# Kernel tuning notes

Hardware: AMD Instinct MI355X
Metric: run time of the kernel (lower is better)

Reference implementation:

```python
import jax, jax.numpy as jnp
import numpy as np

WARMUP = 5

def _smooth_l1(x):
    a = jnp.abs(x)
    return jnp.where(a < 1.0, 0.5 * a * a, a - 0.5)


def setup_inputs() -> dict:
    key = jax.random.key(0)
    ks = jax.random.split(key, 6)
    B, S, N, M, C = 8, 4, 8192, 50, 10
    return dict(
        pred_boxes=jax.random.normal(ks[0], (B, S, N, 7), jnp.float32),
        pred_classes=jax.random.normal(ks[1], (B, S, N, C), jnp.float32),
        pred_scores=jax.random.normal(ks[2], (B, S, N), jnp.float32),
        gt_boxes=jax.random.normal(ks[3], (B, M, 7), jnp.float32) * 3.0,
        gt_classes=jax.random.randint(ks[4], (B, M), 0, C),
        n_gt=jax.random.randint(ks[5], (B,), 1, M + 1),
        w_center=jnp.float32(2.0),   # loss_weights['center']
        w_obj=jnp.float32(0.5),      # loss_weights['obj']
        w_unmatched=jnp.float32(5.0),# loss_weights['unmatched']
        epoch=0,
    )


def _forward(pred_boxes, pred_classes, pred_scores, gt_boxes, gt_classes, n_gt, w_center, w_obj, w_unmatched, epoch):
    # epoch < WARMUP path: k_factor=10, use_objectness=False, distance_threshold=5.0, cls_weight=0
    K_FACTOR = 10
    COST_THRESH = 5.0 * 10.0  # distance_threshold * 10
    B, S, N, _ = pred_boxes.shape
    M = gt_boxes.shape[1]
    gt_mask = jnp.arange(M)[None, :] < n_gt[:, None]            # [B,M] valid (non-padded) GTs

    pc = pred_boxes[..., :3]                                    # [B,S,N,3]
    gc = gt_boxes[..., :3]                                      # [B,M,3]
    diff = pc[:, :, :, None, :] - gc[:, None, None, :, :]       # [B,S,N,M,3]
    dist = jnp.sqrt(jnp.sum(diff * diff, axis=-1))              # [B,S,N,M] center L2 cost

    # ---- progressive matching (vectorized over B,S,GT) ----
    cost = jnp.where(gt_mask[:, None, None, :], dist, jnp.inf)
    masked = jnp.where(cost < COST_THRESH, cost, jnp.inf)
    neg = -jnp.swapaxes(masked, -1, -2)                         # [B,S,M,N]
    vals, idx = jax.lax.top_k(neg, K_FACTOR)                    # k smallest costs per gt
    pick_ok = vals > -jnp.inf                                   # [B,S,M,k] valid picks
    gt_ids = jnp.broadcast_to(jnp.arange(M, dtype=jnp.int32)[None, None, :, None], idx.shape)
    bidx = jnp.broadcast_to(jnp.arange(B)[:, None, None, None], idx.shape)
    sidx = jnp.broadcast_to(jnp.arange(S)[None, :, None, None], idx.shape)
    assign = jnp.full((B, S, N), -1, dtype=jnp.int32)
    assign = assign.at[bidx, sidx, idx].max(jnp.where(pick_ok, gt_ids, -1))
    matched_gt = pick_ok.any(-1)                                # [B,S,M]
    unmatched = gt_mask[:, None, :] & ~matched_gt               # [B,S,M]

    # ---- center loss (smooth-L1 over matched query/GT center pairs) ----
    pos = assign >= 0                                           # [B,S,N]
    a = jnp.maximum(assign, 0)
    gtc = gc[jnp.arange(B)[:, None, None], a]                   # [B,S,N,3]
    n_pos = pos.sum().astype(jnp.float32)
    loss_center = jnp.sum(_smooth_l1(pc - gtc) * pos[..., None]) / jnp.maximum(n_pos * 3.0, 1.0)

    # ---- progressive objectness loss (BCE-with-logits + dynamic pos_weight) ----
    t = pos.astype(pred_scores.dtype)
    n_neg = jnp.float32(t.size) - n_pos
    pw = jnp.minimum(10.0, n_neg / jnp.maximum(n_pos, 1.0))     # epoch < warmup branch
    x = pred_scores
    loss_obj = jnp.mean(pw * t * jax.nn.softplus(-x) + (1.0 - t) * jax.nn.softplus(x))

    # ---- unmatched-GT loss: pull 5 nearest predictions toward each unmatched GT ----
    dist_t = jnp.swapaxes(dist, -1, -2)                         # [B,S,M,N]
    nd, ni = jax.lax.top_k(-dist_t, 5)
    nd = -nd                                                    # 5 smallest distances [B,S,M,5]
    b5 = jnp.broadcast_to(jnp.arange(B)[:, None, None, None], ni.shape)
    s5 = jnp.broadcast_to(jnp.arange(S)[None, :, None, None], ni.shape)
    obj5 = pred_scores[b5, s5, ni]                              # [B,S,M,5]
    per_gt = jnp.mean(jnp.exp(-nd / 2.0) * (1.0 - obj5), axis=-1)
    per_gt = jnp.where(unmatched, per_gt, 0.0)
    n_entries = jnp.sum(unmatched.any(-1)).astype(jnp.float32)  # number of (b,s) pairs with unmatched gts
    loss_unm = per_gt.sum() / jnp.maximum(n_entries, 1.0)

    return loss_center * w_center + loss_obj * w_obj + loss_unm * w_unmatched


def reference(pred_boxes, pred_classes, pred_scores, gt_boxes, gt_classes, n_gt, w_center, w_obj, w_unmatched, epoch):
    return _forward(pred_boxes, pred_classes, pred_scores, gt_boxes, gt_classes, n_gt, w_center, w_obj, w_unmatched, epoch)
```

## Files before the change

### kernel.cpp

```cpp
#include <hip/hip_runtime.h>

#define NB 8
#define NS 4
#define NN 8192
#define NM 50
#define K10 10
#define COST_THRESH 50.0f
#define LOSS_BLOCKS 256
#define CAP 1024
#define CAP_HI 128
#define TOTAL (NB * NS * NN)
#define TT 512
#define ELEMS (NN / TT)

__device__ __forceinline__ bool lexless(float d1, int i1, float d2, int i2) {
  return (d1 < d2) || (d1 == d2 && i1 < i2);
}

__global__ void __launch_bounds__(256) prep_kernel(
    const float* __restrict__ pred_boxes, float* __restrict__ packed,
    int* __restrict__ assign, float* __restrict__ acc,
    int* __restrict__ bs_unm, int* __restrict__ done) {
  int i = blockIdx.x * blockDim.x + threadIdx.x;
  for (int j = i; j < TOTAL; j += gridDim.x * blockDim.x) {
    assign[j] = -1;
    packed[j] = pred_boxes[j * 7 + 0];
    packed[TOTAL + j] = pred_boxes[j * 7 + 1];
    packed[2 * TOTAL + j] = pred_boxes[j * 7 + 2];
  }
  if (i == 0) { acc[0] = 0.0f; *done = 0; }
  if (i >= 64 && i < 64 + NB * NS) bs_unm[i - 64] = 0;
}

__global__ void __launch_bounds__(TT, 4) topk_kernel(
    const float* __restrict__ packed, const float* __restrict__ pred_scores,
    const float* __restrict__ gt_boxes, const int* __restrict__ n_gt,
    int* __restrict__ assign, float* __restrict__ per_gt_sum,
    int* __restrict__ bs_unm) {
  const int blk = blockIdx.x;
  const int m = blk % NM;
  const int bs = blk / NM;
  const int b = bs / NS;
  const int t = threadIdx.x;
  const int wave = t >> 6;
  const int lane = t & 63;

  __shared__ float scd[CAP];
  __shared__ int sci[CAP];
  __shared__ float sred[2][8];
  __shared__ float sbb[2];
  __shared__ int scount[2][8];
  __shared__ int scnt;
  __shared__ float soutd[K10];
  __shared__ int souti[K10];

  if (t == 0) scnt = 0;

  const float gx = gt_boxes[(b * NM + m) * 7 + 0];
  const float gy = gt_boxes[(b * NM + m) * 7 + 1];
  const float gz = gt_boxes[(b * NM + m) * 7 + 2];
  const bool valid = (m < n_gt[b]);

  const float4* px4 = (const float4*)(packed + (size_t)bs * NN);
  const float4* py4 = (const float4*)(packed + TOTAL + (size_t)bs * NN);
  const float4* pz4 = (const float4*)(packed + 2 * TOTAL + (size_t)bs * NN);

  float d2r[ELEMS];
  float lmin = INFINITY, lmax = 0.0f;
#pragma unroll
  for (int c = 0; c < ELEMS / 4; c++) {
    float4 vx = px4[c * TT + t];
    float4 vy = py4[c * TT + t];
    float4 vz = pz4[c * TT + t];
    float dx, dy, dz;
    dx = vx.x - gx; dy = vy.x - gy; dz = vz.x - gz; d2r[c * 4 + 0] = dx * dx + dy * dy + dz * dz;
    dx = vx.y - gx; dy = vy.y - gy; dz = vz.y - gz; d2r[c * 4 + 1] = dx * dx + dy * dy + dz * dz;
    dx = vx.z - gx; dy = vy.z - gy; dz = vz.z - gz; d2r[c * 4 + 2] = dx * dx + dy * dy + dz * dz;
    dx = vx.w - gx; dy = vy.w - gy; dz = vz.w - gz; d2r[c * 4 + 3] = dx * dx + dy * dy + dz * dz;
#pragma unroll
    for (int j = 0; j < 4; j++) {
      lmin = fminf(lmin, d2r[c * 4 + j]);
      lmax = fmaxf(lmax, d2r[c * 4 + j]);
    }
  }
#pragma unroll
  for (int off = 32; off >= 1; off >>= 1) {
    lmin = fminf(lmin, __shfl_down(lmin, off));
    lmax = fmaxf(lmax, __shfl_down(lmax, off));
  }
  if (lane == 0) { sred[0][wave] = lmin; sred[1][wave] = lmax; }
  __syncthreads();
  if (t == 0) {
    float bmin = INFINITY, bmax = 0.0f;
#pragma unroll
    for (int w = 0; w < TT / 64; w++) {
      bmin = fminf(bmin, sred[0][w]);
      bmax = fmaxf(bmax, sred[1][w]);
    }
    sbb[0] = bmin;
    sbb[1] = bmax;
  }
  __syncthreads();

  float lo = sbb[0];
  float hi = sbb[1] * 1.000001f + 1e-30f;
  float bound = hi;
  int buf = 0;
  for (int iter = 0; iter < 32; iter++) {
    float mid = 0.5f * (lo + hi);
    int c = 0;
#pragma unroll
    for (int e = 0; e < ELEMS; e++) c += (d2r[e] < mid) ? 1 : 0;
#pragma unroll
    for (int off = 32; off >= 1; off >>= 1) c += __shfl_down(c, off);
    if (lane == 0) scount[buf][wave] = c;
    __syncthreads();
    int C = 0;
#pragma unroll
    for (int w = 0; w < TT / 64; w++) C += scount[buf][w];
    buf ^= 1;
    bool collapsed = (mid <= lo) || (mid >= hi);
    if (C >= K10 && (C <= CAP_HI || collapsed)) { bound = mid; break; }
    if (collapsed) { bound = hi; break; }
    if (C < K10) lo = mid; else hi = mid;
  }

#pragma unroll
  for (int e = 0; e < ELEMS; e++) {
    int n = (e < ELEMS ? ((e >> 2) * TT + t) * 4 + (e & 3) : 0);
    bool p = d2r[e] < bound;
    unsigned long long mask = __ballot(p);
    if (mask) {
      int leader = __ffsll((long long)mask) - 1;
      int cnt = __popcll(mask);
      int base = 0;
      if (lane == leader) base = atomicAdd(&scnt, cnt);
      base = __shfl(base, leader);
      int pos = base + __popcll(mask & ((1ull << lane) - 1ull));
      if (p && pos < CAP) { scd[pos] = d2r[e]; sci[pos] = n; }
    }
  }
  __syncthreads();
  const int K = min(scnt, CAP);

  for (int c = t; c < K; c += TT) scd[c] = sqrtf(scd[c]);
  __syncthreads();
  for (int c = t; c < K; c += TT) {
    float dc = scd[c];
    int ic = sci[c];
    int rank = 0;
    for (int o = 0; o < K; o++) rank += lexless(scd[o], sci[o], dc, ic) ? 1 : 0;
    if (rank < K10) { soutd[rank] = dc; souti[rank] = ic; }
  }
  __syncthreads();

  if (t < 64) {
    bool pick = (t < K10) && valid && (soutd[t] < COST_THRESH);
    if (pick) atomicMax(&assign[(size_t)bs * NN + souti[t]], m);
    bool matched = __any(pick);
    if (valid && !matched) {
      float a = 0.0f;
      if (t < 5) a = expf(-0.5f * soutd[t]) * (1.0f - pred_scores[(size_t)bs * NN + souti[t]]);
#pragma unroll
      for (int off = 8; off >= 1; off >>= 1) a += __shfl_down(a, off);
      if (t == 0) {
        atomicAdd(per_gt_sum, a * 0.2f);
        atomicOr(&bs_unm[bs], 1);
      }
    }
  }
}

__global__ void __launch_bounds__(256) loss_final_kernel(
    const float* __restrict__ packed, const float* __restrict__ pred_scores,
    const float* __restrict__ gt_boxes, const int* __restrict__ assign,
    float* __restrict__ partials, int* __restrict__ done,
    const float* __restrict__ acc, const int* __restrict__ bs_unm,
    const float* __restrict__ wc, const float* __restrict__ wo,
    const float* __restrict__ wu, float* __restrict__ out) {
  int tid = blockIdx.x * blockDim.x + threadIdx.x;
  float lc = 0.0f, spp = 0.0f, spn = 0.0f, np = 0.0f;
  for (int i = tid; i < TOTAL; i += gridDim.x * blockDim.x) {
    int a = assign[i];
    float x = pred_scores[i];
    if (a >= 0) {
      np += 1.0f;
      int b = i / (NS * NN);
      const float* gbp = &gt_boxes[(b * NM + a) * 7];
#pragma unroll
      for (int c = 0; c < 3; c++) {
        float diff = packed[c * TOTAL + i] - gbp[c];
        float ad = fabsf(diff);
        lc += (ad < 1.0f) ? 0.5f * ad * ad : (ad - 0.5f);
      }
      spp += log1pf(expf(-fabsf(x))) + fmaxf(-x, 0.0f);
    } else {
      spn += log1pf(expf(-fabsf(x))) + fmaxf(x, 0.0f);
    }
  }
#pragma unroll
  for (int off = 32; off >= 1; off >>= 1) {
    lc += __shfl_down(lc, off);
    spp += __shfl_down(spp, off);
    spn += __shfl_down(spn, off);
    np += __shfl_down(np, off);
  }
  __shared__ float red[4][4];
  __shared__ int s_last;
  int wave = threadIdx.x >> 6;
  if ((threadIdx.x & 63) == 0) {
    red[wave][0] = lc; red[wave][1] = spp; red[wave][2] = spn; red[wave][3] = np;
  }
  __syncthreads();
  if (threadIdx.x == 0) {
    float o0 = 0, o1 = 0, o2 = 0, o3 = 0;
#pragma unroll
    for (int w = 0; w < 4; w++) { o0 += red[w][0]; o1 += red[w][1]; o2 += red[w][2]; o3 += red[w][3]; }
    float* p = &partials[(size_t)blockIdx.x * 8];
    __hip_atomic_store(&p[0], o0, __ATOMIC_RELAXED, __HIP_MEMORY_SCOPE_AGENT);
    __hip_atomic_store(&p[1], o1, __ATOMIC_RELAXED, __HIP_MEMORY_SCOPE_AGENT);
    __hip_atomic_store(&p[2], o2, __ATOMIC_RELAXED, __HIP_MEMORY_SCOPE_AGENT);
    __hip_atomic_store(&p[3], o3, __ATOMIC_RELAXED, __HIP_MEMORY_SCOPE_AGENT);
    __threadfence();
    int ticket = __hip_atomic_fetch_add(done, 1, __ATOMIC_ACQ_REL, __HIP_MEMORY_SCOPE_AGENT);
    s_last = (ticket == gridDim.x - 1) ? 1 : 0;
  }
  __syncthreads();
  if (s_last) {
    __threadfence();
    const int t = threadIdx.x;
    float l0 = __hip_atomic_load(&partials[t * 8 + 0], __ATOMIC_RELAXED, __HIP_MEMORY_SCOPE_AGENT);
    float l1 = __hip_atomic_load(&partials[t * 8 + 1], __ATOMIC_RELAXED, __HIP_MEMORY_SCOPE_AGENT);
    float l2 = __hip_atomic_load(&partials[t * 8 + 2], __ATOMIC_RELAXED, __HIP_MEMORY_SCOPE_AGENT);
    float l3 = __hip_atomic_load(&partials[t * 8 + 3], __ATOMIC_RELAXED, __HIP_MEMORY_SCOPE_AGENT);
#pragma unroll
    for (int off = 32; off >= 1; off >>= 1) {
      l0 += __shfl_down(l0, off);
      l1 += __shfl_down(l1, off);
      l2 += __shfl_down(l2, off);
      l3 += __shfl_down(l3, off);
    }
    __shared__ float red2[4][4];
    if ((t & 63) == 0) {
      red2[t >> 6][0] = l0; red2[t >> 6][1] = l1; red2[t >> 6][2] = l2; red2[t >> 6][3] = l3;
    }
    __syncthreads();
    if (t == 0) {
      float o0 = 0, o1 = 0, o2 = 0, o3 = 0;
#pragma unroll
      for (int w = 0; w < 4; w++) { o0 += red2[w][0]; o1 += red2[w][1]; o2 += red2[w][2]; o3 += red2[w][3]; }
      int ne = 0;
      for (int i = 0; i < NB * NS; i++) ne += bs_unm[i];
      float n_pos = o3;
      float loss_center = o0 / fmaxf(n_pos * 3.0f, 1.0f);
      float n_neg = (float)TOTAL - n_pos;
      float pw = fminf(10.0f, n_neg / fmaxf(n_pos, 1.0f));
      float loss_obj = (pw * o1 + o2) / (float)TOTAL;
      float loss_unm = acc[0] / fmaxf((float)ne, 1.0f);
      out[0] = loss_center * wc[0] + loss_obj * wo[0] + loss_unm * wu[0];
    }
  }
}

extern "C" void kernel_launch(void* const* d_in, const int* in_sizes, int n_in,
                              void* d_out, int out_size, void* d_ws, size_t ws_size,
                              hipStream_t stream) {
  const float* pred_boxes = (const float*)d_in[0];
  const float* pred_scores = (const float*)d_in[2];
  const float* gt_boxes = (const float*)d_in[3];
  const int* n_gt = (const int*)d_in[5];
  const float* wc = (const float*)d_in[6];
  const float* wo = (const float*)d_in[7];
  const float* wu = (const float*)d_in[8];
  float* out = (float*)d_out;

  char* ws = (char*)d_ws;
  int* assign = (int*)ws;
  float* packed = (float*)(ws + (size_t)TOTAL * 4);
  float* acc = (float*)(ws + (size_t)TOTAL * 16);
  int* done = (int*)((char*)acc + 64);
  int* bs_unm = (int*)((char*)acc + 128);
  float* partials = (float*)((char*)acc + 512);

  prep_kernel<<<512, 256, 0, stream>>>(pred_boxes, packed, assign, acc, bs_unm, done);
  topk_kernel<<<NB * NS * NM, TT, 0, stream>>>(packed, pred_scores, gt_boxes,
                                               n_gt, assign, &acc[0], bs_unm);
  loss_final_kernel<<<LOSS_BLOCKS, 256, 0, stream>>>(packed, pred_scores, gt_boxes, assign,
                                                     partials, done, acc, bs_unm, wc, wo, wu, out);
}
```

Baseline: 53.63 us.

## Move assignment to per-(b,s) shared-memory scatter and use galloping threshold search

The top-k kernel now only writes each GT's 10 nearest (distance, index) pairs to a small buffer. The loss kernel runs one block group per (batch, sample) and builds the assignment map in LDS with shared atomics, so the global assign array, its initialisation and the global atomics are gone. The unmatched-GT loss is folded into that kernel. The threshold search now starts from a geometric gallop above the minimum with a looser accept window, and the top-k block shrinks to 256 threads with 32 elements each. The trade-offs are a larger candidate buffer, a possibly bigger rank-sort set, and only 128 loss blocks, each rebuilding the same LDS assignment.

After: 47.49 us. 11.4% less time.

```diff
diff --git a/kernel.cpp b/kernel.cpp
--- a/kernel.cpp
+++ b/kernel.cpp
@@ -6,12 +6,14 @@
 #define NM 50
 #define K10 10
 #define COST_THRESH 50.0f
-#define LOSS_BLOCKS 256
-#define CAP 1024
-#define CAP_HI 128
 #define TOTAL (NB * NS * NN)
-#define TT 512
-#define ELEMS (NN / TT)
+#define TKT 256
+#define TKE 32
+#define CAP 2048
+#define ACCEPT 256
+#define LFT 512
+#define SUBS 4
+#define LF_BLOCKS (NB * NS * SUBS)
 
 __device__ __forceinline__ bool lexless(float d1, int i1, float d2, int i2) {
   return (d1 < d2) || (d1 == d2 && i1 < i2);
@@ -19,24 +21,19 @@
 
 __global__ void __launch_bounds__(256) prep_kernel(
     const float* __restrict__ pred_boxes, float* __restrict__ packed,
-    int* __restrict__ assign, float* __restrict__ acc,
-    int* __restrict__ bs_unm, int* __restrict__ done) {
+    int* __restrict__ done) {
   int i = blockIdx.x * blockDim.x + threadIdx.x;
   for (int j = i; j < TOTAL; j += gridDim.x * blockDim.x) {
-    assign[j] = -1;
     packed[j] = pred_boxes[j * 7 + 0];
     packed[TOTAL + j] = pred_boxes[j * 7 + 1];
     packed[2 * TOTAL + j] = pred_boxes[j * 7 + 2];
   }
-  if (i == 0) { acc[0] = 0.0f; *done = 0; }
-  if (i >= 64 && i < 64 + NB * NS) bs_unm[i - 64] = 0;
-}
-
-__global__ void __launch_bounds__(TT, 4) topk_kernel(
-    const float* __restrict__ packed, const float* __restrict__ pred_scores,
-    const float* __restrict__ gt_boxes, const int* __restrict__ n_gt,
-    int* __restrict__ assign, float* __restrict__ per_gt_sum,
-    int* __restrict__ bs_unm) {
+  if (i == 0) *done = 0;
+}
+
+__global__ void __launch_bounds__(TKT, 4) topk_kernel(
+    const float* __restrict__ packed, const float* __restrict__ gt_boxes,
+    float* __restrict__ outd, int* __restrict__ outi) {
   const int blk = blockIdx.x;
   const int m = blk % NM;
   const int bs = blk / NM;
@@ -47,9 +44,8 @@
 
   __shared__ float scd[CAP];
   __shared__ int sci[CAP];
-  __shared__ float sred[2][8];
-  __shared__ float sbb[2];
-  __shared__ int scount[2][8];
+  __shared__ float sred[2][4];
+  __shared__ int scount[2][4];
   __shared__ int scnt;
   __shared__ float soutd[K10];
   __shared__ int souti[K10];
@@ -59,19 +55,18 @@
   const float gx = gt_boxes[(b * NM + m) * 7 + 0];
   const float gy = gt_boxes[(b * NM + m) * 7 + 1];
   const float gz = gt_boxes[(b * NM + m) * 7 + 2];
-  const bool valid = (m < n_gt[b]);
 
   const float4* px4 = (const float4*)(packed + (size_t)bs * NN);
   const float4* py4 = (const float4*)(packed + TOTAL + (size_t)bs * NN);
   const float4* pz4 = (const float4*)(packed + 2 * TOTAL + (size_t)bs * NN);
 
-  float d2r[ELEMS];
+  float d2r[TKE];
   float lmin = INFINITY, lmax = 0.0f;
 #pragma unroll
-  for (int c = 0; c < ELEMS / 4; c++) {
-    float4 vx = px4[c * TT + t];
-    float4 vy = py4[c * TT + t];
-    float4 vz = pz4[c * TT + t];
+  for (int c = 0; c < TKE / 4; c++) {
+    float4 vx = px4[c * TKT + t];
+    float4 vy = py4[c * TKT + t];
+    float4 vz = pz4[c * TKT + t];
     float dx, dy, dz;
     dx = vx.x - gx; dy = vy.x - gy; dz = vz.x - gz; d2r[c * 4 + 0] = dx * dx + dy * dy + dz * dz;
     dx = vx.y - gx; dy = vy.y - gy; dz = vz.y - gz; d2r[c * 4 + 1] = dx * dx + dy * dy + dz * dz;
@@ -90,44 +85,39 @@
   }
   if (lane == 0) { sred[0][wave] = lmin; sred[1][wave] = lmax; }
   __syncthreads();
-  if (t == 0) {
-    float bmin = INFINITY, bmax = 0.0f;
-#pragma unroll
-    for (int w = 0; w < TT / 64; w++) {
-      bmin = fminf(bmin, sred[0][w]);
-      bmax = fmaxf(bmax, sred[1][w]);
-    }
-    sbb[0] = bmin;
-    sbb[1] = bmax;
-  }
-  __syncthreads();
-
-  float lo = sbb[0];
-  float hi = sbb[1] * 1.000001f + 1e-30f;
-  float bound = hi;
+  const float bmin = fminf(fminf(sred[0][0], sred[0][1]), fminf(sred[0][2], sred[0][3]));
+  const float bmax = fmaxf(fmaxf(sred[1][0], sred[1][1]), fmaxf(sred[1][2], sred[1][3]));
+
+  float lo = bmin;
+  float hi = bmax * 1.000001f + 1e-30f;
+  float g = fmaxf(bmin * 4.0f, 1e-37f);
+  bool have = false;
   int buf = 0;
-  for (int iter = 0; iter < 32; iter++) {
-    float mid = 0.5f * (lo + hi);
+  for (int it = 0; it < 24; it++) {
+    float probe = have ? 0.5f * (lo + hi) : fminf(g, hi);
     int c = 0;
 #pragma unroll
-    for (int e = 0; e < ELEMS; e++) c += (d2r[e] < mid) ? 1 : 0;
+    for (int e = 0; e < TKE; e++) c += (d2r[e] < probe) ? 1 : 0;
 #pragma unroll
     for (int off = 32; off >= 1; off >>= 1) c += __shfl_down(c, off);
     if (lane == 0) scount[buf][wave] = c;
     __syncthreads();
-    int C = 0;
-#pragma unroll
-    for (int w = 0; w < TT / 64; w++) C += scount[buf][w];
+    int C = scount[buf][0] + scount[buf][1] + scount[buf][2] + scount[buf][3];
     buf ^= 1;
-    bool collapsed = (mid <= lo) || (mid >= hi);
-    if (C >= K10 && (C <= CAP_HI || collapsed)) { bound = mid; break; }
-    if (collapsed) { bound = hi; break; }
-    if (C < K10) lo = mid; else hi = mid;
-  }
-
-#pragma unroll
-  for (int e = 0; e < ELEMS; e++) {
-    int n = (e < ELEMS ? ((e >> 2) * TT + t) * 4 + (e & 3) : 0);
+    if (C >= K10) {
+      hi = probe; have = true;
+      if (C <= ACCEPT) break;
+    } else {
+      lo = probe;
+      if (!have) { g *= 4.0f; if (g >= hi) have = true; }
+    }
+    if (have && !(hi > lo + fmaxf(lo, 1e-30f) * 1e-7f)) break;
+  }
+  const float bound = hi;
+
+#pragma unroll
+  for (int e = 0; e < TKE; e++) {
+    int n = ((e >> 2) * TKT + t) * 4 + (e & 3);
     bool p = d2r[e] < bound;
     unsigned long long mask = __ballot(p);
     if (mask) {
@@ -143,9 +133,9 @@
   __syncthreads();
   const int K = min(scnt, CAP);
 
-  for (int c = t; c < K; c += TT) scd[c] = sqrtf(scd[c]);
-  __syncthreads();
-  for (int c = t; c < K; c += TT) {
+  for (int c = t; c < K; c += TKT) scd[c] = sqrtf(scd[c]);
+  __syncthreads();
+  for (int c = t; c < K; c += TKT) {
     float dc = scd[c];
     int ic = sci[c];
     int rank = 0;
@@ -154,42 +144,76 @@
   }
   __syncthreads();
 
-  if (t < 64) {
-    bool pick = (t < K10) && valid && (soutd[t] < COST_THRESH);
-    if (pick) atomicMax(&assign[(size_t)bs * NN + souti[t]], m);
-    bool matched = __any(pick);
-    if (valid && !matched) {
-      float a = 0.0f;
-      if (t < 5) a = expf(-0.5f * soutd[t]) * (1.0f - pred_scores[(size_t)bs * NN + souti[t]]);
-#pragma unroll
-      for (int off = 8; off >= 1; off >>= 1) a += __shfl_down(a, off);
-      if (t == 0) {
-        atomicAdd(per_gt_sum, a * 0.2f);
-        atomicOr(&bs_unm[bs], 1);
-      }
-    }
-  }
-}
-
-__global__ void __launch_bounds__(256) loss_final_kernel(
-    const float* __restrict__ packed, const float* __restrict__ pred_scores,
-    const float* __restrict__ gt_boxes, const int* __restrict__ assign,
+  if (t < K10) {
+    outd[blk * K10 + t] = soutd[t];
+    outi[blk * K10 + t] = souti[t];
+  }
+}
+
+__global__ void __launch_bounds__(LFT) loss_final_kernel(
+    const float* __restrict__ pred_boxes, const float* __restrict__ pred_scores,
+    const float* __restrict__ gt_boxes, const int* __restrict__ n_gt,
+    const float* __restrict__ outd, const int* __restrict__ outi,
     float* __restrict__ partials, int* __restrict__ done,
-    const float* __restrict__ acc, const int* __restrict__ bs_unm,
     const float* __restrict__ wc, const float* __restrict__ wo,
     const float* __restrict__ wu, float* __restrict__ out) {
-  int tid = blockIdx.x * blockDim.x + threadIdx.x;
+  const int blk = blockIdx.x;
+  const int bs = blk / SUBS;
+  const int sub = blk % SUBS;
+  const int b = bs / NS;
+  const int t = threadIdx.x;
+  const int wave = t >> 6;
+
+  __shared__ int lassign[NN];
+  __shared__ int matched[NM];
+  __shared__ float spg;
+  __shared__ int sunm;
+  __shared__ float red[8][4];
+  __shared__ float red2[2][8];
+  __shared__ int s_last;
+
+  for (int i = t; i < NN; i += LFT) lassign[i] = -1;
+  if (t < NM) matched[t] = 0;
+  if (t == 0) { spg = 0.0f; sunm = 0; }
+  const int ngt = n_gt[b];
+  __syncthreads();
+
+  if (t < NM * K10) {
+    int m = t / K10, k = t % K10;
+    if (m < ngt) {
+      float d = outd[(bs * NM + m) * K10 + k];
+      if (d < COST_THRESH) {
+        atomicMax(&lassign[outi[(bs * NM + m) * K10 + k]], m);
+        atomicOr(&matched[m], 1);
+      }
+    }
+  }
+  __syncthreads();
+
+  if (sub == 0 && t < NM && t < ngt && matched[t] == 0) {
+    float a = 0.0f;
+#pragma unroll
+    for (int k = 0; k < 5; k++) {
+      float d = outd[(bs * NM + t) * K10 + k];
+      float sc = pred_scores[(size_t)bs * NN + outi[(bs * NM + t) * K10 + k]];
+      a += expf(-0.5f * d) * (1.0f - sc);
+    }
+    atomicAdd(&spg, a * 0.2f);
+    atomicOr(&sunm, 1);
+  }
+
   float lc = 0.0f, spp = 0.0f, spn = 0.0f, np = 0.0f;
-  for (int i = tid; i < TOTAL; i += gridDim.x * blockDim.x) {
-    int a = assign[i];
-    float x = pred_scores[i];
+  const int base = sub * (NN / SUBS);
+#pragma unroll
+  for (int j = 0; j < NN / SUBS / LFT; j++) {
+    int i = base + t + j * LFT;
+    int a = lassign[i];
+    float x = pred_scores[(size_t)bs * NN + i];
     if (a >= 0) {
       np += 1.0f;
-      int b = i / (NS * NN);
-      const float* gbp = &gt_boxes[(b * NM + a) * 7];
 #pragma unroll
       for (int c = 0; c < 3; c++) {
-        float diff = packed[c * TOTAL + i] - gbp[c];
+        float diff = pred_boxes[((size_t)bs * NN + i) * 7 + c] - gt_boxes[(b * NM + a) * 7 + c];
         float ad = fabsf(diff);
         lc += (ad < 1.0f) ? 0.5f * ad * ad : (ad - 0.5f);
       }
@@ -205,58 +229,57 @@
     spn += __shfl_down(spn, off);
     np += __shfl_down(np, off);
   }
-  __shared__ float red[4][4];
-  __shared__ int s_last;
-  int wave = threadIdx.x >> 6;
-  if ((threadIdx.x & 63) == 0) {
+  if ((t & 63) == 0) {
     red[wave][0] = lc; red[wave][1] = spp; red[wave][2] = spn; red[wave][3] = np;
   }
   __syncthreads();
-  if (threadIdx.x == 0) {
+  if (t == 0) {
     float o0 = 0, o1 = 0, o2 = 0, o3 = 0;
 #pragma unroll
-    for (int w = 0; w < 4; w++) { o0 += red[w][0]; o1 += red[w][1]; o2 += red[w][2]; o3 += red[w][3]; }
-    float* p = &partials[(size_t)blockIdx.x * 8];
+    for (int w = 0; w < 8; w++) { o0 += red[w][0]; o1 += red[w][1]; o2 += red[w][2]; o3 += red[w][3]; }
+    float* p = &partials[(size_t)blk * 8];
     __hip_atomic_store(&p[0], o0, __ATOMIC_RELAXED, __HIP_MEMORY_SCOPE_AGENT);
     __hip_atomic_store(&p[1], o1, __ATOMIC_RELAXED, __HIP_MEMORY_SCOPE_AGENT);
     __hip_atomic_store(&p[2], o2, __ATOMIC_RELAXED, __HIP_MEMORY_SCOPE_AGENT);
     __hip_atomic_store(&p[3], o3, __ATOMIC_RELAXED, __HIP_MEMORY_SCOPE_AGENT);
+    __hip_atomic_store(&p[4], sub == 0 ? spg : 0.0f, __ATOMIC_RELAXED, __HIP_MEMORY_SCOPE_AGENT);
+    __hip_atomic_store(&p[5], sub == 0 ? (float)sunm : 0.0f, __ATOMIC_RELAXED, __HIP_MEMORY_SCOPE_AGENT);
     __threadfence();
     int ticket = __hip_atomic_fetch_add(done, 1, __ATOMIC_ACQ_REL, __HIP_MEMORY_SCOPE_AGENT);
-    s_last = (ticket == gridDim.x - 1) ? 1 : 0;
+    s_last = (ticket == LF_BLOCKS - 1) ? 1 : 0;
   }
   __syncthreads();
   if (s_last) {
     __threadfence();
-    const int t = threadIdx.x;
-    float l0 = __hip_atomic_load(&partials[t * 8 + 0], __ATOMIC_RELAXED, __HIP_MEMORY_SCOPE_AGENT);
-    float l1 = __hip_atomic_load(&partials[t * 8 + 1], __ATOMIC_RELAXED, __HIP_MEMORY_SCOPE_AGENT);
-    float l2 = __hip_atomic_load(&partials[t * 8 + 2], __ATOMIC_RELAXED, __HIP_MEMORY_SCOPE_AGENT);
-    float l3 = __hip_atomic_load(&partials[t * 8 + 3], __ATOMIC_RELAXED, __HIP_MEMORY_SCOPE_AGENT);
+    float v[6] = {0, 0, 0, 0, 0, 0};
+    if (t < LF_BLOCKS) {
+#pragma unroll
+      for (int q = 0; q < 6; q++)
+        v[q] = __hip_atomic_load(&partials[(size_t)t * 8 + q], __ATOMIC_RELAXED, __HIP_MEMORY_SCOPE_AGENT);
+    }
 #pragma unroll
     for (int off = 32; off >= 1; off >>= 1) {
-      l0 += __shfl_down(l0, off);
-      l1 += __shfl_down(l1, off);
-      l2 += __shfl_down(l2, off);
-      l3 += __shfl_down(l3, off);
-    }
-    __shared__ float red2[4][4];
-    if ((t & 63) == 0) {
-      red2[t >> 6][0] = l0; red2[t >> 6][1] = l1; red2[t >> 6][2] = l2; red2[t >> 6][3] = l3;
+#pragma unroll
+      for (int q = 0; q < 6; q++) v[q] += __shfl_down(v[q], off);
+    }
+    if (t < 128 && (t & 63) == 0) {
+#pragma unroll
+      for (int q = 0; q < 6; q++) red2[t >> 6][q] = v[q];
     }
     __syncthreads();
     if (t == 0) {
-      float o0 = 0, o1 = 0, o2 = 0, o3 = 0;
-#pragma unroll
-      for (int w = 0; w < 4; w++) { o0 += red2[w][0]; o1 += red2[w][1]; o2 += red2[w][2]; o3 += red2[w][3]; }
-      int ne = 0;
-      for (int i = 0; i < NB * NS; i++) ne += bs_unm[i];
+      float o0 = red2[0][0] + red2[1][0];
+      float o1 = red2[0][1] + red2[1][1];
+      float o2 = red2[0][2] + red2[1][2];
+      float o3 = red2[0][3] + red2[1][3];
+      float pg = red2[0][4] + red2[1][4];
+      float ne = red2[0][5] + red2[1][5];
       float n_pos = o3;
       float loss_center = o0 / fmaxf(n_pos * 3.0f, 1.0f);
       float n_neg = (float)TOTAL - n_pos;
       float pw = fminf(10.0f, n_neg / fmaxf(n_pos, 1.0f));
       float loss_obj = (pw * o1 + o2) / (float)TOTAL;
-      float loss_unm = acc[0] / fmaxf((float)ne, 1.0f);
+      float loss_unm = pg / fmaxf(ne, 1.0f);
       out[0] = loss_center * wc[0] + loss_obj * wo[0] + loss_unm * wu[0];
     }
   }
@@ -275,16 +298,14 @@
   float* out = (float*)d_out;
 
   char* ws = (char*)d_ws;
-  int* assign = (int*)ws;
-  float* packed = (float*)(ws + (size_t)TOTAL * 4);
-  float* acc = (float*)(ws + (size_t)TOTAL * 16);
-  int* done = (int*)((char*)acc + 64);
-  int* bs_unm = (int*)((char*)acc + 128);
-  float* partials = (float*)((char*)acc + 512);
-
-  prep_kernel<<<512, 256, 0, stream>>>(pred_boxes, packed, assign, acc, bs_unm, done);
-  topk_kernel<<<NB * NS * NM, TT, 0, stream>>>(packed, pred_scores, gt_boxes,
-                                               n_gt, assign, &acc[0], bs_unm);
-  loss_final_kernel<<<LOSS_BLOCKS, 256, 0, stream>>>(packed, pred_scores, gt_boxes, assign,
-                                                     partials, done, acc, bs_unm, wc, wo, wu, out);
-}
+  float* packed = (float*)ws;
+  float* outd = (float*)(ws + (size_t)TOTAL * 12);
+  int* outi = (int*)((char*)outd + (size_t)NB * NS * NM * K10 * 4);
+  float* partials = (float*)((char*)outi + (size_t)NB * NS * NM * K10 * 4);
+  int* done = (int*)((char*)partials + LF_BLOCKS * 8 * 4 + 64);
+
+  prep_kernel<<<512, 256, 0, stream>>>(pred_boxes, packed, done);
+  topk_kernel<<<NB * NS * NM, TKT, 0, stream>>>(packed, gt_boxes, outd, outi);
+  loss_final_kernel<<<LF_BLOCKS, LFT, 0, stream>>>(pred_boxes, pred_scores, gt_boxes, n_gt,
+                                                   outd, outi, partials, done, wc, wo, wu, out);
+}
```
